# Kernel tuning notes

Measured on AMD Instinct MI355X. Metric: run time of the kernel, lower is better.

## Reference

```python
import jax, jax.numpy as jnp
import numpy as np

K = 1024      # num_embeddings
D = 256       # embedding_dim
BETA = 0.25


def setup_inputs() -> dict:
    key = jax.random.key(0)
    k1, k2 = jax.random.split(key)
    z = jax.random.normal(k1, (4, D, 16, 32, 32), dtype=jnp.float32)
    # matches torch init: uniform(-1/K, 1/K)
    embedding = jax.random.uniform(k2, (K, D), dtype=jnp.float32,
                                   minval=-1.0 / K, maxval=1.0 / K)
    return {"z": z, "embedding": embedding}


def reference(z, embedding):
    # z: (B, C, Dd, H, W) with C == D
    z_perm = jnp.transpose(z, (0, 2, 3, 4, 1))          # (B, Dd, H, W, C)
    flat = z_perm.reshape(-1, D)                        # (N, D)

    dist = (jnp.sum(flat * flat, axis=1, keepdims=True)
            + jnp.sum(embedding * embedding, axis=1)
            - 2.0 * flat @ embedding.T)
    indices_flat = jnp.argmin(dist, axis=1)             # (N,)

    # one-hot @ embedding == direct gather
    z_q_flat = embedding[indices_flat]                  # (N, D)
    z_q = z_q_flat.reshape(z_perm.shape)

    commitment_loss = jnp.mean((z_perm - jax.lax.stop_gradient(z_q)) ** 2)
    vq_loss = BETA * commitment_loss

    # straight-through estimator
    z_q_st = z_perm + jax.lax.stop_gradient(z_q - z_perm)
    z_q_out = jnp.transpose(z_q_st, (0, 4, 1, 2, 3))    # back to (B, C, Dd, H, W)

    # perplexity from assignment histogram
    n = flat.shape[0]
    counts = jnp.zeros((K,), dtype=flat.dtype).at[indices_flat].add(1.0)
    avg_probs = counts / n
    perplexity = jnp.exp(-jnp.sum(avg_probs * jnp.log(avg_probs + 1e-10)))

    indices = indices_flat.reshape(z_perm.shape[:-1])   # (B, Dd, H, W)
    return z_q_out, vq_loss, indices, perplexity
```

## Files before the change

### kernel.cpp

```cpp
#include <hip/hip_runtime.h>

#define Dd 256
#define Kc 1024
#define SPATIAL 16384
#define NROWS 65536
#define NELEM 16777216
#define LOSS_OFF 16777216
#define IDX_OFF  16777217
#define PERP_OFF (16777217 + 65536)
#define MARGIN 3.5e-4f
#define SCSTRIDE 1048

typedef _Float16 f16x8 __attribute__((ext_vector_type(8)));
typedef float f32x4 __attribute__((ext_vector_type(4)));


__global__ __launch_bounds__(256) void prep2_kernel(const float* __restrict__ emb,
                                                    _Float16* __restrict__ efp,
                                                    float* __restrict__ se) {
  const int j = blockIdx.x, c = threadIdx.x;
  float v = emb[j * Dd + c];
  const int ct2 = j >> 4, l15 = j & 15;
  const int kk = c >> 5, q = (c >> 3) & 3, e = c & 7;
  efp[((size_t)(ct2 * 8 + kk) * 64 + q * 16 + l15) * 8 + e] = (_Float16)(v * 1024.0f);
  double s = (double)v * (double)v;
  #pragma unroll
  for (int off = 32; off; off >>= 1) s += __shfl_down(s, off, 64);
  __shared__ double ws4[4];
  if ((threadIdx.x & 63) == 0) ws4[threadIdx.x >> 6] = s;
  __syncthreads();
  if (threadIdx.x == 0) se[j] = (float)(ws4[0] + ws4[1] + ws4[2] + ws4[3]);
}

__global__ __launch_bounds__(512, 4) void prefilter2_kernel(const float* __restrict__ z,
                                                            const _Float16* __restrict__ efp,
                                                            const float* __restrict__ se,
                                                            float* __restrict__ sx,
                                                            int* __restrict__ candcount,
                                                            int* __restrict__ cand_g,
                                                            float* __restrict__ out_idx_f,
                                                            int* __restrict__ idx_i,
                                                            int* __restrict__ counts,
                                                            int* __restrict__ hardcnt,
                                                            int* __restrict__ hardlist,
                                                            double* __restrict__ loss_sum) {
  __shared__ __align__(16) _Float16 scAs[32 * SCSTRIDE];
  __shared__ double sxp[16][32];
  __shared__ float selds[Kc];
  __shared__ int cnts[32];
  __shared__ int cands[32][8];
  __shared__ float rminw[8][32];
  __shared__ float rthr[32];

  const int tid = threadIdx.x;
  const int n0 = blockIdx.x * 32;
  const int b = n0 >> 14, s0 = n0 & 16383;
  const float* zb = z + (size_t)b * (Dd * SPATIAL) + s0;

  {
    const int r = tid & 31, cp = tid >> 5;
    double acc = 0.0;
    #pragma unroll
    for (int c = cp * 16; c < cp * 16 + 16; ++c) {
      const float v = zb[(size_t)c * SPATIAL + r];
      scAs[r * 272 + c] = (_Float16)v;
      acc += (double)v * (double)v;
    }
    sxp[cp][r] = acc;
  }
  selds[tid] = se[tid];
  selds[tid + 512] = se[tid + 512];
  if (tid < 32) cnts[tid] = 0;
  __syncthreads();

  float sxv = 0.0f;
  if (tid < 32) {
    double s = 0.0;
    #pragma unroll
    for (int p = 0; p < 16; ++p) s += sxp[p][tid];
    sxv = (float)s;
    sx[n0 + tid] = sxv;
  }

  const int w = tid >> 6, lane = tid & 63, q = lane >> 4, l15 = lane & 15;
  const int colbase = w * 128;

  f16x8 Afrag[2][8];
  #pragma unroll
  for (int rt = 0; rt < 2; ++rt)
    #pragma unroll
    for (int kk = 0; kk < 8; ++kk)
      Afrag[rt][kk] = *(const f16x8*)(&scAs[(rt * 16 + l15) * 272 + kk * 32 + q * 8]);

  __syncthreads();

  float rmin8[8];
  #pragma unroll
  for (int i = 0; i < 8; ++i) rmin8[i] = 3.4e38f;

  #pragma unroll
  for (int ct = 0; ct < 8; ++ct) {
    const _Float16* bp = efp + ((size_t)((w * 8 + ct) * 8) * 64 + lane) * 8;
    f32x4 a0 = {0.f, 0.f, 0.f, 0.f}, a1 = {0.f, 0.f, 0.f, 0.f};
    #pragma unroll
    for (int kk = 0; kk < 8; ++kk) {
      const f16x8 B = *(const f16x8*)(bp + kk * 512);
      a0 = __builtin_amdgcn_mfma_f32_16x16x32_f16(Afrag[0][kk], B, a0, 0, 0, 0);
      a1 = __builtin_amdgcn_mfma_f32_16x16x32_f16(Afrag[1][kk], B, a1, 0, 0, 0);
    }
    const int col = colbase + ct * 16 + l15;
    const float sec = selds[col];
    #pragma unroll
    for (int reg = 0; reg < 4; ++reg) {
      const float sc0 = fmaf(-0.001953125f, a0[reg], sec);
      const float sc1 = fmaf(-0.001953125f, a1[reg], sec);
      rmin8[reg]     = fminf(rmin8[reg], sc0);
      rmin8[reg + 4] = fminf(rmin8[reg + 4], sc1);
      scAs[(q * 4 + reg) * SCSTRIDE + col]      = (_Float16)sc0;
      scAs[(16 + q * 4 + reg) * SCSTRIDE + col] = (_Float16)sc1;
    }
  }

  #pragma unroll
  for (int m = 1; m <= 8; m <<= 1)
    #pragma unroll
    for (int i = 0; i < 8; ++i) rmin8[i] = fminf(rmin8[i], __shfl_xor(rmin8[i], m, 64));
  if (l15 == 0) {
    #pragma unroll
    for (int reg = 0; reg < 4; ++reg) {
      rminw[w][q * 4 + reg] = rmin8[reg];
      rminw[w][16 + q * 4 + reg] = rmin8[4 + reg];
    }
  }
  __syncthreads();

  float rm1 = 0.0f;
  if (tid < 32) {
    float m = rminw[0][tid];
    #pragma unroll
    for (int ww = 1; ww < 8; ++ww) m = fminf(m, rminw[ww][tid]);
    rm1 = m;
    rthr[tid] = m + MARGIN;
  }
  __syncthreads();

  {
    const int row = tid >> 4, t4 = tid & 15;
    const float thr = rthr[row];
    #pragma unroll
    for (int i = 0; i < 8; ++i) {
      const f16x8 v = *(const f16x8*)(&scAs[row * SCSTRIDE + t4 * 8 + i * 128]);
      #pragma unroll
      for (int e = 0; e < 8; ++e) {
        if ((float)v[e] < thr) {
          const int pos = atomicAdd(&cnts[row], 1);
          if (pos < 8) cands[row][pos] = t4 * 8 + i * 128 + e;
        }
      }
    }
  }
  __syncthreads();

  if (tid < 256)
    cand_g[(size_t)(n0 + (tid >> 3)) * 8 + (tid & 7)] = cands[tid >> 3][tid & 7];
  if (tid < 64) {
    double lp = 0.0;
    int hard = 0;
    const int n = n0 + tid;
    if (tid < 32) {
      const int cnt = cnts[tid];
      candcount[n] = cnt;
      if (cnt == 1) {
        const int j = cands[tid][0];
        idx_i[n] = j;
        out_idx_f[n] = (float)j;
        atomicAdd(&counts[j], 1);
        lp = (double)sxv + (double)rm1;
      } else {
        hard = 1;
      }
    }
    const unsigned long long mask = __ballot(hard);
    const int h = __popcll(mask);
    int base = 0;
    if (tid == 0 && h) base = atomicAdd(hardcnt, h);
    base = __shfl(base, 0, 64);
    if (hard) {
      const int rank = __popcll(mask & ((1ull << tid) - 1ull));
      hardlist[base + rank] = n;
    }
    #pragma unroll
    for (int off = 32; off; off >>= 1) lp += __shfl_down(lp, off, 64);
    if (tid == 0 && lp != 0.0) atomicAdd(loss_sum, lp);
  }
}

__global__ __launch_bounds__(256) void resolve_hard_kernel(const float* __restrict__ z,
                                                           const float* __restrict__ emb,
                                                           const float* __restrict__ se,
                                                           const float* __restrict__ sx,
                                                           const int* __restrict__ candcount,
                                                           const int* __restrict__ cand_g,
                                                           const int* __restrict__ hardcnt,
                                                           const int* __restrict__ hardlist,
                                                           float* __restrict__ out_idx_f,
                                                           int* __restrict__ idx_i,
                                                           int* __restrict__ counts,
                                                           double* __restrict__ loss_sum) {
  __shared__ float xs[4][256];
  const int tid = threadIdx.x, w = tid >> 6, lane = tid & 63;
  const int hc = *hardcnt;
  const int nw = gridDim.x * 4;
  double wloss = 0.0;
  for (int i = blockIdx.x * 4 + w; i < hc; i += nw) {
    const int n = hardlist[i];
    const int b = n >> 14, s = n & 16383;
    #pragma unroll
    for (int ro = 0; ro < 4; ++ro)
      xs[w][ro * 64 + lane] =
          z[(size_t)b * (Dd * SPATIAL) + (size_t)(ro * 64 + lane) * SPATIAL + s];
    asm volatile("s_waitcnt lgkmcnt(0) vmcnt(0)" ::: "memory");
    const int cnt = candcount[n];
    const float sxn = sx[n];
    float scb = 3.4e38f;
    int jb = 0x7fffffff;
    if (cnt <= 8) {
      if (lane < cnt) {
        jb = cand_g[(size_t)n * 8 + lane];
        const float4* ep = (const float4*)(emb + (size_t)jb * Dd);
        float acc = 0.f;
        #pragma unroll 8
        for (int kk = 0; kk < 64; ++kk) {
          const float4 e4 = ep[kk];
          const float* xp = &xs[w][kk * 4];
          acc = fmaf(xp[0], e4.x, acc);
          acc = fmaf(xp[1], e4.y, acc);
          acc = fmaf(xp[2], e4.z, acc);
          acc = fmaf(xp[3], e4.w, acc);
        }
        const float t1 = sxn + se[jb];
        scb = t1 - 2.0f * acc;
      }
    } else {
      for (int jj = 0; jj < 16; ++jj) {
        const int j = lane * 16 + jj;
        const float4* ep = (const float4*)(emb + (size_t)j * Dd);
        float acc = 0.f;
        #pragma unroll 8
        for (int kk = 0; kk < 64; ++kk) {
          const float4 e4 = ep[kk];
          const float* xp = &xs[w][kk * 4];
          acc = fmaf(xp[0], e4.x, acc);
          acc = fmaf(xp[1], e4.y, acc);
          acc = fmaf(xp[2], e4.z, acc);
          acc = fmaf(xp[3], e4.w, acc);
        }
        const float t1 = sxn + se[j];
        const float sc = t1 - 2.0f * acc;
        if (sc < scb) { scb = sc; jb = j; }
      }
    }
    #pragma unroll
    for (int m = 1; m <= 32; m <<= 1) {
      const float so = __shfl_xor(scb, m, 64);
      const int jo = __shfl_xor(jb, m, 64);
      if (so < scb || (so == scb && jo < jb)) { scb = so; jb = jo; }
    }
    if (lane == 0) {
      idx_i[n] = jb;
      out_idx_f[n] = (float)jb;
      atomicAdd(&counts[jb], 1);
      wloss += (double)sxn + (double)scb;
    }
  }
  if (lane == 0) atomicAdd(loss_sum, wloss);
}

__global__ __launch_bounds__(256) void phase2c_kernel(const float* __restrict__ emb,
                                                      const int* __restrict__ idx_i,
                                                      float* __restrict__ out_zq) {
  __shared__ float els[64 * 257];
  __shared__ int sidx[64];
  const int tid = threadIdx.x;
  const int blk = blockIdx.x, b = blk >> 8, s0 = (blk & 255) << 6;
  if (tid < 64) sidx[tid] = idx_i[b * SPATIAL + s0 + tid];
  __syncthreads();
  {
    const int rr = tid >> 2, p = tid & 3;
    const float* ep = emb + (size_t)sidx[rr] * Dd + p * 64;
    float* dl = els + rr * 257 + p * 64;
    #pragma unroll
    for (int i = 0; i < 64; i += 4) {
      const float4 e4 = *(const float4*)(ep + i);
      dl[i] = e4.x; dl[i + 1] = e4.y; dl[i + 2] = e4.z; dl[i + 3] = e4.w;
    }
  }
  __syncthreads();
  const int s4 = tid & 15, cg = tid >> 4;
  const size_t zb = (size_t)b * (Dd * SPATIAL);
  #pragma unroll 4
  for (int c = cg; c < Dd; c += 16) {
    float4 v;
    v.x = els[(s4 * 4 + 0) * 257 + c];
    v.y = els[(s4 * 4 + 1) * 257 + c];
    v.z = els[(s4 * 4 + 2) * 257 + c];
    v.w = els[(s4 * 4 + 3) * 257 + c];
    *(float4*)(out_zq + zb + (size_t)c * SPATIAL + s0 + s4 * 4) = v;
  }
}

__global__ __launch_bounds__(256) void finalize_kernel(const int* __restrict__ counts,
                                                       const double* __restrict__ loss_sum,
                                                       float* __restrict__ out) {
  const int tid = threadIdx.x;
  double local = 0.0;
  for (int k = tid; k < Kc; k += 256) {
    const double p = (double)counts[k] / (double)NROWS;
    local += p * log(p + 1e-10);
  }
  #pragma unroll
  for (int off = 32; off; off >>= 1) local += __shfl_down(local, off, 64);
  __shared__ double dred[4];
  if ((tid & 63) == 0) dred[tid >> 6] = local;
  __syncthreads();
  if (tid == 0) {
    const double H = dred[0] + dred[1] + dred[2] + dred[3];
    out[PERP_OFF] = (float)exp(-H);
    out[LOSS_OFF] = (float)(0.25 * loss_sum[0] / (double)NELEM);
  }
}


__global__ __launch_bounds__(256) void prep_kernel(const float* __restrict__ emb,
                                                   float* __restrict__ eT,
                                                   float* __restrict__ se) {
  const int j = blockIdx.x, c = threadIdx.x;
  float v = emb[j * Dd + c];
  eT[c * Kc + j] = v;
  double s = (double)v * (double)v;
  #pragma unroll
  for (int off = 32; off; off >>= 1) s += __shfl_down(s, off, 64);
  __shared__ double ws4[4];
  if ((threadIdx.x & 63) == 0) ws4[threadIdx.x >> 6] = s;
  __syncthreads();
  if (threadIdx.x == 0) se[j] = (float)(ws4[0] + ws4[1] + ws4[2] + ws4[3]);
}

__global__ __launch_bounds__(256) void sx_kernel(const float* __restrict__ z,
                                                 float* __restrict__ sx) {
  __shared__ double part[4][64];
  const int tid = threadIdx.x, r = tid & 63, cg = tid >> 6;
  const int blk = blockIdx.x, b = blk >> 8, s0 = (blk & 255) << 6;
  const float* zb = z + (size_t)b * (Dd * SPATIAL);
  double acc = 0.0;
  for (int c = cg * 64; c < cg * 64 + 64; ++c) {
    const float v = zb[(size_t)c * SPATIAL + s0 + r];
    acc += (double)v * (double)v;
  }
  part[cg][r] = acc;
  __syncthreads();
  if (tid < 64)
    sx[b * SPATIAL + s0 + tid] =
        (float)(part[0][tid] + part[1][tid] + part[2][tid] + part[3][tid]);
}

__global__ __launch_bounds__(256) void argmin_kernel(const float* __restrict__ z,
                                                     const float* __restrict__ eT,
                                                     const float* __restrict__ se,
                                                     const float* __restrict__ sx,
                                                     float* __restrict__ out_idx_f,
                                                     int* __restrict__ idx_i,
                                                     int* __restrict__ counts) {
  __shared__ float As[32 * 64];
  __shared__ float Bs[32 * 64];
  __shared__ float ses[Kc];
  __shared__ float sxs[64];
  __shared__ float redS1[64 * 16];
  __shared__ int   redI1[64 * 16];
  const int tid = threadIdx.x, tc = tid & 15, tr = tid >> 4;
  const int blk = blockIdx.x, b = blk >> 8, s0 = (blk & 255) << 6;
  const float* zb = z + (size_t)b * (Dd * SPATIAL);
  #pragma unroll
  for (int i = 0; i < 4; ++i) ses[tid + 256 * i] = se[tid + 256 * i];
  if (tid < 64) sxs[tid] = sx[b * SPATIAL + s0 + tid];
  float s1[4]; int j1[4];
  #pragma unroll
  for (int r = 0; r < 4; ++r) { s1[r] = 3.4e38f; j1[r] = 0; }
  for (int j0 = 0; j0 < Kc; j0 += 64) {
    float acc[4][4];
    #pragma unroll
    for (int rr = 0; rr < 4; ++rr)
      #pragma unroll
      for (int cc = 0; cc < 4; ++cc) acc[rr][cc] = 0.0f;
    for (int c0 = 0; c0 < Dd; c0 += 32) {
      __syncthreads();
      #pragma unroll
      for (int i = 0; i < 8; ++i) {
        const int e = i * 256 + tid, ci = e >> 6, r = e & 63;
        As[e] = zb[(size_t)(c0 + ci) * SPATIAL + s0 + r];
        Bs[e] = eT[(c0 + ci) * Kc + j0 + r];
      }
      __syncthreads();
      #pragma unroll
      for (int d = 0; d < 32; ++d) {
        const float4 av = *reinterpret_cast<const float4*>(&As[d * 64 + 4 * tr]);
        const float4 bv = *reinterpret_cast<const float4*>(&Bs[d * 64 + 4 * tc]);
        const float aa[4] = {av.x, av.y, av.z, av.w};
        const float bb[4] = {bv.x, bv.y, bv.z, bv.w};
        #pragma unroll
        for (int rr = 0; rr < 4; ++rr)
          #pragma unroll
          for (int cc = 0; cc < 4; ++cc)
            acc[rr][cc] = fmaf(aa[rr], bb[cc], acc[rr][cc]);
      }
    }
    #pragma unroll
    for (int rr = 0; rr < 4; ++rr) {
      const float sxr = sxs[4 * tr + rr];
      #pragma unroll
      for (int cc = 0; cc < 4; ++cc) {
        const int j = j0 + 4 * tc + cc;
        const float t1 = sxr + ses[j];
        const float s = t1 - 2.0f * acc[rr][cc];
        if (s < s1[rr] || (s == s1[rr] && j < j1[rr])) { s1[rr] = s; j1[rr] = j; }
      }
    }
  }
  #pragma unroll
  for (int rr = 0; rr < 4; ++rr) {
    redS1[(4 * tr + rr) * 16 + tc] = s1[rr];
    redI1[(4 * tr + rr) * 16 + tc] = j1[rr];
  }
  __syncthreads();
  if (tid < 64) {
    float bs = redS1[tid * 16];
    int bj = redI1[tid * 16];
    #pragma unroll
    for (int t = 1; t < 16; ++t) {
      const float a1 = redS1[tid * 16 + t];
      const int aj = redI1[tid * 16 + t];
      if (a1 < bs || (a1 == bs && aj < bj)) { bs = a1; bj = aj; }
    }
    const int n = b * SPATIAL + s0 + tid;
    out_idx_f[n] = (float)bj;
    idx_i[n] = bj;
    atomicAdd(&counts[bj], 1);
  }
}

__global__ __launch_bounds__(256) void phase2_kernel(const float* __restrict__ z,
                                                     const float* __restrict__ eT,
                                                     const int* __restrict__ idx_i,
                                                     float* __restrict__ out_zq,
                                                     double* __restrict__ loss_sum) {
  __shared__ int sidx[64];
  __shared__ double dred[4];
  const int tid = threadIdx.x;
  const int blk = blockIdx.x, b = blk >> 8, s0 = (blk & 255) << 6;
  if (tid < 64) sidx[tid] = idx_i[b * SPATIAL + s0 + tid];
  __syncthreads();
  const int s = tid & 63, coff = tid >> 6;
  const size_t zb = (size_t)b * (Dd * SPATIAL);
  const int myidx = sidx[s];
  double lsum = 0.0;
  for (int c = coff; c < Dd; c += 4) {
    const size_t off = zb + (size_t)c * SPATIAL + s0 + s;
    const float zv = z[off];
    const float zq = eT[c * Kc + myidx];
    out_zq[off] = zv + (zq - zv);
    const float d = zv - zq;
    lsum += (double)d * (double)d;
  }
  #pragma unroll
  for (int off = 32; off; off >>= 1) lsum += __shfl_down(lsum, off, 64);
  if ((tid & 63) == 0) dred[tid >> 6] = lsum;
  __syncthreads();
  if (tid == 0) atomicAdd(loss_sum, dred[0] + dred[1] + dred[2] + dred[3]);
}


extern "C" void kernel_launch(void* const* d_in, const int* in_sizes, int n_in,
                              void* d_out, int out_size, void* d_ws, size_t ws_size,
                              hipStream_t stream) {
  const float* z   = (const float*)d_in[0];
  const float* emb = (const float*)d_in[1];
  float* out = (float*)d_out;
  char* ws = (char*)d_ws;

  const size_t OFF_SE   = 8192;
  const size_t OFF_SX   = 12288;
  const size_t OFF_EF   = 274432;
  const size_t OFF_RM   = 798720;
  const size_t OFF_IDX  = 1060864;
  const size_t OFF_CCT  = 1323008;
  const size_t OFF_CAND = 1585152;
  const size_t OFF_HARD = 3682304;
  const size_t NEED     = 3944448;
  (void)OFF_RM;

  double* loss_sum = (double*)(ws + 0);
  int*    hardcnt  = (int*)(ws + 8);
  int*    counts   = (int*)(ws + 256);

  hipMemsetAsync(d_ws, 0, 8192, stream);

  if (ws_size >= NEED) {
    float*    se        = (float*)(ws + OFF_SE);
    float*    sx        = (float*)(ws + OFF_SX);
    _Float16* efp       = (_Float16*)(ws + OFF_EF);
    int*      idx_i     = (int*)(ws + OFF_IDX);
    int*      candcount = (int*)(ws + OFF_CCT);
    int*      cand_g    = (int*)(ws + OFF_CAND);
    int*      hardlist  = (int*)(ws + OFF_HARD);

    prep2_kernel<<<Kc, 256, 0, stream>>>(emb, efp, se);
    prefilter2_kernel<<<2048, 512, 0, stream>>>(z, efp, se, sx, candcount, cand_g,
                                                out + IDX_OFF, idx_i, counts,
                                                hardcnt, hardlist, loss_sum);
    resolve_hard_kernel<<<256, 256, 0, stream>>>(z, emb, se, sx, candcount, cand_g,
                                                 hardcnt, hardlist, out + IDX_OFF,
                                                 idx_i, counts, loss_sum);
    phase2c_kernel<<<1024, 256, 0, stream>>>(emb, idx_i, out);
    finalize_kernel<<<1, 256, 0, stream>>>(counts, loss_sum, out);
  } else {
    float* eT    = (float*)(ws + 8192);
    float* se    = (float*)(ws + 8192 + 1048576);
    float* sx    = (float*)(ws + 8192 + 1048576 + 4096);
    int*   idx_i = (int*)(ws + 8192 + 1048576 + 4096 + 262144);

    prep_kernel<<<Kc, 256, 0, stream>>>(emb, eT, se);
    sx_kernel<<<1024, 256, 0, stream>>>(z, sx);
    argmin_kernel<<<1024, 256, 0, stream>>>(z, eT, se, sx, out + IDX_OFF, idx_i, counts);
    phase2_kernel<<<1024, 256, 0, stream>>>(z, eT, idx_i, out, loss_sum);
    finalize_kernel<<<1, 256, 0, stream>>>(counts, loss_sum, out);
  }
}
```

Before: 262.9 us.

## Track top-two minima in registers instead of staging scores for candidate scan

The prefilter kernel now keeps a running best and second-best score plus the best column per row in registers, and reduces them across lanes and waves. This replaces writing all fp16 scores to LDS and rescanning them with shared atomics. That shrinks LDS use, which may allow higher occupancy, and drops a pass and two barriers. Rows whose gap between best and second-best is below the margin become hard rows, and those are now always resolved by a full 1024-code fp32 search, since the candidate-list path is gone. The resolve grid is doubled, and the sum of squares switches from double to float accumulation, with some risk of slightly different loss rounding.

New measurement: 809.0 us. 208% more time.

```diff
diff --git a/kernel.cpp b/kernel.cpp
--- a/kernel.cpp
+++ b/kernel.cpp
@@ -9,7 +9,6 @@
 #define IDX_OFF  16777217
 #define PERP_OFF (16777217 + 65536)
 #define MARGIN 3.5e-4f
-#define SCSTRIDE 1048
 
 typedef _Float16 f16x8 __attribute__((ext_vector_type(8)));
 typedef float f32x4 __attribute__((ext_vector_type(4)));
@@ -36,21 +35,18 @@
                                                             const _Float16* __restrict__ efp,
                                                             const float* __restrict__ se,
                                                             float* __restrict__ sx,
-                                                            int* __restrict__ candcount,
-                                                            int* __restrict__ cand_g,
                                                             float* __restrict__ out_idx_f,
                                                             int* __restrict__ idx_i,
                                                             int* __restrict__ counts,
                                                             int* __restrict__ hardcnt,
                                                             int* __restrict__ hardlist,
                                                             double* __restrict__ loss_sum) {
-  __shared__ __align__(16) _Float16 scAs[32 * SCSTRIDE];
-  __shared__ double sxp[16][32];
+  __shared__ _Float16 As[32 * 272];
+  __shared__ float sxp[16][32];
   __shared__ float selds[Kc];
-  __shared__ int cnts[32];
-  __shared__ int cands[32][8];
-  __shared__ float rminw[8][32];
-  __shared__ float rthr[32];
+  __shared__ float rm1w[8][32];
+  __shared__ float rm2w[8][32];
+  __shared__ int   rc1w[8][32];
 
   const int tid = threadIdx.x;
   const int n0 = blockIdx.x * 32;
@@ -59,27 +55,26 @@
 
   {
     const int r = tid & 31, cp = tid >> 5;
-    double acc = 0.0;
+    float acc = 0.0f;
     #pragma unroll
     for (int c = cp * 16; c < cp * 16 + 16; ++c) {
       const float v = zb[(size_t)c * SPATIAL + r];
-      scAs[r * 272 + c] = (_Float16)v;
-      acc += (double)v * (double)v;
+      As[r * 272 + c] = (_Float16)v;
+      acc = fmaf(v, v, acc);
     }
     sxp[cp][r] = acc;
   }
   selds[tid] = se[tid];
   selds[tid + 512] = se[tid + 512];
-  if (tid < 32) cnts[tid] = 0;
   __syncthreads();
 
   float sxv = 0.0f;
   if (tid < 32) {
-    double s = 0.0;
+    float s = 0.0f;
     #pragma unroll
     for (int p = 0; p < 16; ++p) s += sxp[p][tid];
-    sxv = (float)s;
-    sx[n0 + tid] = sxv;
+    sxv = s;
+    sx[n0 + tid] = s;
   }
 
   const int w = tid >> 6, lane = tid & 63, q = lane >> 4, l15 = lane & 15;
@@ -90,13 +85,12 @@
   for (int rt = 0; rt < 2; ++rt)
     #pragma unroll
     for (int kk = 0; kk < 8; ++kk)
-      Afrag[rt][kk] = *(const f16x8*)(&scAs[(rt * 16 + l15) * 272 + kk * 32 + q * 8]);
-
-  __syncthreads();
-
-  float rmin8[8];
-  #pragma unroll
-  for (int i = 0; i < 8; ++i) rmin8[i] = 3.4e38f;
+      Afrag[rt][kk] = *(const f16x8*)(&As[(rt * 16 + l15) * 272 + kk * 32 + q * 8]);
+
+  float m1[8], m2[8];
+  int   c1[8];
+  #pragma unroll
+  for (int i = 0; i < 8; ++i) { m1[i] = 3.4e38f; m2[i] = 3.4e38f; c1[i] = 0; }
 
   #pragma unroll
   for (int ct = 0; ct < 8; ++ct) {
@@ -114,68 +108,58 @@
     for (int reg = 0; reg < 4; ++reg) {
       const float sc0 = fmaf(-0.001953125f, a0[reg], sec);
       const float sc1 = fmaf(-0.001953125f, a1[reg], sec);
-      rmin8[reg]     = fminf(rmin8[reg], sc0);
-      rmin8[reg + 4] = fminf(rmin8[reg + 4], sc1);
-      scAs[(q * 4 + reg) * SCSTRIDE + col]      = (_Float16)sc0;
-      scAs[(16 + q * 4 + reg) * SCSTRIDE + col] = (_Float16)sc1;
-    }
-  }
-
-  #pragma unroll
-  for (int m = 1; m <= 8; m <<= 1)
-    #pragma unroll
-    for (int i = 0; i < 8; ++i) rmin8[i] = fminf(rmin8[i], __shfl_xor(rmin8[i], m, 64));
+      m2[reg] = fminf(m2[reg], fmaxf(m1[reg], sc0));
+      c1[reg] = (sc0 < m1[reg]) ? col : c1[reg];
+      m1[reg] = fminf(m1[reg], sc0);
+      m2[4 + reg] = fminf(m2[4 + reg], fmaxf(m1[4 + reg], sc1));
+      c1[4 + reg] = (sc1 < m1[4 + reg]) ? col : c1[4 + reg];
+      m1[4 + reg] = fminf(m1[4 + reg], sc1);
+    }
+  }
+
+  #pragma unroll
+  for (int m = 1; m <= 8; m <<= 1) {
+    #pragma unroll
+    for (int i = 0; i < 8; ++i) {
+      const float om1 = __shfl_xor(m1[i], m, 64);
+      const float om2 = __shfl_xor(m2[i], m, 64);
+      const int   oc1 = __shfl_xor(c1[i], m, 64);
+      m2[i] = fminf(fminf(m2[i], om2), fmaxf(m1[i], om1));
+      if (om1 < m1[i]) { m1[i] = om1; c1[i] = oc1; }
+    }
+  }
   if (l15 == 0) {
     #pragma unroll
     for (int reg = 0; reg < 4; ++reg) {
-      rminw[w][q * 4 + reg] = rmin8[reg];
-      rminw[w][16 + q * 4 + reg] = rmin8[4 + reg];
-    }
-  }
-  __syncthreads();
-
-  float rm1 = 0.0f;
-  if (tid < 32) {
-    float m = rminw[0][tid];
-    #pragma unroll
-    for (int ww = 1; ww < 8; ++ww) m = fminf(m, rminw[ww][tid]);
-    rm1 = m;
-    rthr[tid] = m + MARGIN;
-  }
-  __syncthreads();
-
-  {
-    const int row = tid >> 4, t4 = tid & 15;
-    const float thr = rthr[row];
-    #pragma unroll
-    for (int i = 0; i < 8; ++i) {
-      const f16x8 v = *(const f16x8*)(&scAs[row * SCSTRIDE + t4 * 8 + i * 128]);
-      #pragma unroll
-      for (int e = 0; e < 8; ++e) {
-        if ((float)v[e] < thr) {
-          const int pos = atomicAdd(&cnts[row], 1);
-          if (pos < 8) cands[row][pos] = t4 * 8 + i * 128 + e;
-        }
-      }
-    }
-  }
-  __syncthreads();
-
-  if (tid < 256)
-    cand_g[(size_t)(n0 + (tid >> 3)) * 8 + (tid & 7)] = cands[tid >> 3][tid & 7];
+      rm1w[w][q * 4 + reg] = m1[reg];
+      rm2w[w][q * 4 + reg] = m2[reg];
+      rc1w[w][q * 4 + reg] = c1[reg];
+      rm1w[w][16 + q * 4 + reg] = m1[4 + reg];
+      rm2w[w][16 + q * 4 + reg] = m2[4 + reg];
+      rc1w[w][16 + q * 4 + reg] = c1[4 + reg];
+    }
+  }
+  __syncthreads();
+
   if (tid < 64) {
     double lp = 0.0;
     int hard = 0;
     const int n = n0 + tid;
     if (tid < 32) {
-      const int cnt = cnts[tid];
-      candcount[n] = cnt;
-      if (cnt == 1) {
-        const int j = cands[tid][0];
-        idx_i[n] = j;
-        out_idx_f[n] = (float)j;
-        atomicAdd(&counts[j], 1);
-        lp = (double)sxv + (double)rm1;
+      float bm1 = rm1w[0][tid], bm2 = rm2w[0][tid];
+      int   bc1 = rc1w[0][tid];
+      #pragma unroll
+      for (int ww = 1; ww < 8; ++ww) {
+        const float a1v = rm1w[ww][tid], a2v = rm2w[ww][tid];
+        const int   ac = rc1w[ww][tid];
+        bm2 = fminf(fminf(bm2, a2v), fmaxf(bm1, a1v));
+        if (a1v < bm1) { bm1 = a1v; bc1 = ac; }
+      }
+      if (bm2 >= bm1 + MARGIN) {
+        idx_i[n] = bc1;
+        out_idx_f[n] = (float)bc1;
+        atomicAdd(&counts[bc1], 1);
+        lp = (double)sxv + (double)bm1;
       } else {
         hard = 1;
       }
@@ -199,8 +183,6 @@
                                                            const float* __restrict__ emb,
                                                            const float* __restrict__ se,
                                                            const float* __restrict__ sx,
-                                                           const int* __restrict__ candcount,
-                                                           const int* __restrict__ cand_g,
                                                            const int* __restrict__ hardcnt,
                                                            const int* __restrict__ hardlist,
                                                            float* __restrict__ out_idx_f,
@@ -220,45 +202,25 @@
       xs[w][ro * 64 + lane] =
           z[(size_t)b * (Dd * SPATIAL) + (size_t)(ro * 64 + lane) * SPATIAL + s];
     asm volatile("s_waitcnt lgkmcnt(0) vmcnt(0)" ::: "memory");
-    const int cnt = candcount[n];
     const float sxn = sx[n];
     float scb = 3.4e38f;
     int jb = 0x7fffffff;
-    if (cnt <= 8) {
-      if (lane < cnt) {
-        jb = cand_g[(size_t)n * 8 + lane];
-        const float4* ep = (const float4*)(emb + (size_t)jb * Dd);
-        float acc = 0.f;
-        #pragma unroll 8
-        for (int kk = 0; kk < 64; ++kk) {
-          const float4 e4 = ep[kk];
-          const float* xp = &xs[w][kk * 4];
-          acc = fmaf(xp[0], e4.x, acc);
-          acc = fmaf(xp[1], e4.y, acc);
-          acc = fmaf(xp[2], e4.z, acc);
-          acc = fmaf(xp[3], e4.w, acc);
-        }
-        const float t1 = sxn + se[jb];
-        scb = t1 - 2.0f * acc;
-      }
-    } else {
-      for (int jj = 0; jj < 16; ++jj) {
-        const int j = lane * 16 + jj;
-        const float4* ep = (const float4*)(emb + (size_t)j * Dd);
-        float acc = 0.f;
-        #pragma unroll 8
-        for (int kk = 0; kk < 64; ++kk) {
-          const float4 e4 = ep[kk];
-          const float* xp = &xs[w][kk * 4];
-          acc = fmaf(xp[0], e4.x, acc);
-          acc = fmaf(xp[1], e4.y, acc);
-          acc = fmaf(xp[2], e4.z, acc);
-          acc = fmaf(xp[3], e4.w, acc);
-        }
-        const float t1 = sxn + se[j];
-        const float sc = t1 - 2.0f * acc;
-        if (sc < scb) { scb = sc; jb = j; }
-      }
+    for (int jj = 0; jj < 16; ++jj) {
+      const int j = lane * 16 + jj;
+      const float4* ep = (const float4*)(emb + (size_t)j * Dd);
+      float acc = 0.f;
+      #pragma unroll 8
+      for (int kk = 0; kk < 64; ++kk) {
+        const float4 e4 = ep[kk];
+        const float* xp = &xs[w][kk * 4];
+        acc = fmaf(xp[0], e4.x, acc);
+        acc = fmaf(xp[1], e4.y, acc);
+        acc = fmaf(xp[2], e4.z, acc);
+        acc = fmaf(xp[3], e4.w, acc);
+      }
+      const float t1 = sxn + se[j];
+      const float sc = t1 - 2.0f * acc;
+      if (sc < scb) { scb = sc; jb = j; }
     }
     #pragma unroll
     for (int m = 1; m <= 32; m <<= 1) {
@@ -490,13 +452,9 @@
   const size_t OFF_SE   = 8192;
   const size_t OFF_SX   = 12288;
   const size_t OFF_EF   = 274432;
-  const size_t OFF_RM   = 798720;
   const size_t OFF_IDX  = 1060864;
-  const size_t OFF_CCT  = 1323008;
-  const size_t OFF_CAND = 1585152;
   const size_t OFF_HARD = 3682304;
   const size_t NEED     = 3944448;
-  (void)OFF_RM;
 
   double* loss_sum = (double*)(ws + 0);
   int*    hardcnt  = (int*)(ws + 8);
@@ -509,15 +467,13 @@
     float*    sx        = (float*)(ws + OFF_SX);
     _Float16* efp       = (_Float16*)(ws + OFF_EF);
     int*      idx_i     = (int*)(ws + OFF_IDX);
-    int*      candcount = (int*)(ws + OFF_CCT);
-    int*      cand_g    = (int*)(ws + OFF_CAND);
     int*      hardlist  = (int*)(ws + OFF_HARD);
 
     prep2_kernel<<<Kc, 256, 0, stream>>>(emb, efp, se);
-    prefilter2_kernel<<<2048, 512, 0, stream>>>(z, efp, se, sx, candcount, cand_g,
+    prefilter2_kernel<<<2048, 512, 0, stream>>>(z, efp, se, sx,
                                                 out + IDX_OFF, idx_i, counts,
                                                 hardcnt, hardlist, loss_sum);
-    resolve_hard_kernel<<<256, 256, 0, stream>>>(z, emb, se, sx, candcount, cand_g,
+    resolve_hard_kernel<<<512, 256, 0, stream>>>(z, emb, se, sx,
                                                  hardcnt, hardlist, out + IDX_OFF,
                                                  idx_i, counts, loss_sum);
     phase2c_kernel<<<1024, 256, 0, stream>>>(emb, idx_i, out);
```
